# Kernel optimization log

Hardware: AMD Instinct MI355X
Metric: run time of the kernel (lower is better)

The kernel has to match this reference:

```python
import jax, jax.numpy as jnp
import numpy as np

# Dims: C = 8*8*4 = 256 input channels, O = 8*8*8 = 512 output channels,
# space_rank = 4, TT ranks = (4, 16, 16).

def setup_inputs() -> dict:
    key = jax.random.key(0)
    ks = jax.random.split(key, 6)
    inp = jax.random.normal(ks[0], (32, 256, 32, 32), dtype=jnp.float32)
    # space_factor: (space_rank, 1, kH, kW)
    space_factor = jax.random.normal(ks[1], (4, 1, 3, 3), dtype=jnp.float32) * 0.3
    # factors[i]: (in_i, rank_i, rank_{i+1}, out_i)
    factor0 = jax.random.normal(ks[2], (8, 4, 16, 8), dtype=jnp.float32) * 0.1
    factor1 = jax.random.normal(ks[3], (8, 16, 16, 8), dtype=jnp.float32) * 0.08
    # last_factor: (in_last, rank_last, out_last)
    last_factor = jax.random.normal(ks[4], (4, 16, 8), dtype=jnp.float32) * 0.1
    bias = jax.random.uniform(ks[5], (512,), dtype=jnp.float32, minval=-0.02, maxval=0.02)
    return {"input": inp, "space_factor": space_factor, "factor0": factor0,
            "factor1": factor1, "last_factor": last_factor, "bias": bias}


def reference(input, space_factor, factor0, factor1, last_factor, bias):
    B, C, H, W = input.shape
    sr = space_factor.shape[0]
    # Depthwise conv: each of the C channels convolved with the same
    # `space_rank` filters (torch repeat along out-channel dim + groups=C).
    w = jnp.tile(space_factor, (C, 1, 1, 1))  # (C*sr, 1, kH, kW)
    y = jax.lax.conv_general_dilated(
        input, w, window_strides=(1, 1), padding=[(1, 1), (1, 1)],
        feature_group_count=C,
        dimension_numbers=("NCHW", "OIHW", "NCHW"))  # (B, C*sr, H', W')
    Hp, Wp = y.shape[2], y.shape[3]
    # (B, n0, n1, n2, sr, H', W') with (n0,n1,n2) = input_chanel_shape
    t = y.reshape(B, 8, 8, 4, sr, Hp, Wp)
    # Contract the tiny TT cores first (optimal order found by tn.contractors.optimal):
    # chain: (n0, n1, n2, r0, o0, o1, o2) -- only ~0.5M elements.
    chain = jnp.einsum("apqx,bqry,crz->abcpxyz", factor0, factor1, last_factor)
    # One big contraction over (n0, n1, n2, r0): effectively a GEMM
    # (B*H'*W', C*sr) x (C*sr, O).
    out = jnp.einsum("nabcphw,abcpxyz->nxyzhw", t, chain)
    out = out.reshape(B, 512, Hp, Wp)
    return out + bias[None, :, None, None]
```

## Files before the change

### kernel.cpp

```cpp
#include <hip/hip_runtime.h>

typedef unsigned short ushort_t;
typedef __attribute__((ext_vector_type(8))) short bf16x8;
typedef __attribute__((ext_vector_type(8))) unsigned short ushort8;
typedef __attribute__((ext_vector_type(4))) float f32x4;

__device__ __forceinline__ unsigned short f2bf(float f) {
  union { float f; unsigned u; } x; x.f = f;
  unsigned r = x.u + 0x7FFFu + ((x.u >> 16) & 1u);
  return (unsigned short)(r >> 16);
}

__global__ __launch_bounds__(256) void chain_kernel(const float* __restrict__ f0,
                                                    const float* __restrict__ f1,
                                                    const float* __restrict__ lf,
                                                    ushort_t* __restrict__ chainT) {
  __shared__ float gs[512];
  int o = blockIdx.x;
  int z = o & 7, y = (o >> 3) & 7, x = o >> 6;
  int tid = threadIdx.x;
  #pragma unroll
  for (int i = 0; i < 2; ++i) {
    int e = tid + i * 256;
    int c = e & 3, q = (e >> 2) & 15, b = e >> 6;
    float s = 0.f;
    #pragma unroll
    for (int r = 0; r < 16; ++r)
      s += f1[((b * 16 + q) * 16 + r) * 8 + y] * lf[(c * 16 + r) * 8 + z];
    gs[e] = s;
  }
  __syncthreads();
  #pragma unroll
  for (int j = 0; j < 4; ++j) {
    int k = tid + j * 256;
    int p = k & 3, c = (k >> 2) & 3, b = (k >> 4) & 7, a = k >> 7;
    float s = 0.f;
    #pragma unroll
    for (int q = 0; q < 16; ++q)
      s += f0[((a * 4 + p) * 16 + q) * 8 + x] * gs[(b * 16 + q) * 4 + c];
    chainT[(size_t)o * 1024 + k] = f2bf(s);
  }
}

__global__ __launch_bounds__(256) void conv_kernel(const float* __restrict__ in,
                                                   const float* __restrict__ sf,
                                                   ushort_t* __restrict__ t) {
  __shared__ float in_lds[64][244];
  __shared__ float sf_l[36];
  int bid = blockIdx.x;
  int cq = bid & 3, h4 = (bid >> 2) & 7, n = bid >> 5;
  int h0 = h4 * 4;
  int tid = threadIdx.x;
  if (tid < 36) sf_l[tid] = sf[tid];
  for (int e = tid; e < 384; e += 256) {
    int ch = e / 6, r = e % 6;
    in_lds[ch][r * 40 + 3] = 0.f;
    in_lds[ch][r * 40 + 36] = 0.f;
  }
  const float* inb = in + ((size_t)n * 256 + cq * 64) * 1024;
  #pragma unroll
  for (int i = 0; i < 12; ++i) {
    int e = tid + i * 256;
    int ch = e / 48, rem = e % 48;
    int r = rem >> 3, w4 = rem & 7;
    int hh = h0 - 1 + r;
    float4 v = make_float4(0.f, 0.f, 0.f, 0.f);
    if (hh >= 0 && hh < 32)
      v = *(const float4*)&inb[(size_t)ch * 1024 + hh * 32 + w4 * 4];
    *(float4*)&in_lds[ch][r * 40 + 4 + w4 * 4] = v;
  }
  __syncthreads();
  float sfr[36];
  #pragma unroll
  for (int i = 0; i < 36; ++i) sfr[i] = sf_l[i];
  int w = tid >> 3, gg = tid & 7;
  size_t m0 = (size_t)n * 1024 + (size_t)h0 * 32 + w;
  #pragma unroll
  for (int j = 0; j < 4; ++j) {
    float acc[4][2][4];
    #pragma unroll
    for (int b = 0; b < 2; ++b) {
      int ch = j * 16 + gg * 2 + b;
      float vals[6][3];
      #pragma unroll
      for (int r = 0; r < 6; ++r)
        #pragma unroll
        for (int dw = 0; dw < 3; ++dw)
          vals[r][dw] = in_lds[ch][r * 40 + 3 + w + dw];
      #pragma unroll
      for (int hh = 0; hh < 4; ++hh)
        #pragma unroll
        for (int p = 0; p < 4; ++p) {
          float s = 0.f;
          #pragma unroll
          for (int dr = 0; dr < 3; ++dr)
            #pragma unroll
            for (int dw = 0; dw < 3; ++dw)
              s += vals[hh + dr][dw] * sfr[p * 9 + dr * 3 + dw];
          acc[hh][b][p] = s;
        }
    }
    #pragma unroll
    for (int hh = 0; hh < 4; ++hh) {
      ushort8 outv;
      #pragma unroll
      for (int b = 0; b < 2; ++b)
        #pragma unroll
        for (int p = 0; p < 4; ++p) outv[b * 4 + p] = f2bf(acc[hh][b][p]);
      *(ushort8*)&t[(m0 + hh * 32) * 1024 + (size_t)(cq * 256 + j * 64 + gg * 8)] = outv;
    }
  }
}

#define AS1 __attribute__((address_space(1)))
#define AS3 __attribute__((address_space(3)))
#define BARRIER  __builtin_amdgcn_s_barrier()
#define LGKMCNT0 asm volatile("s_waitcnt lgkmcnt(0)" ::: "memory")
#define VMCNT4   asm volatile("s_waitcnt vmcnt(4)" ::: "memory")
#define VMCNT0   asm volatile("s_waitcnt vmcnt(0)" ::: "memory")

__global__ __launch_bounds__(512, 2) void gemm_kernel(const ushort_t* __restrict__ tA,
                                                      const ushort_t* __restrict__ tB,
                                                      const float* __restrict__ bias,
                                                      float* __restrict__ out) {
  __shared__ __align__(16) ushort_t smem[65536];
  int tid = threadIdx.x;
  int bid = blockIdx.x;
  int wg = (bid & 7) * 32 + (bid >> 3);
  int tile_m = (wg >> 1) * 256;
  int tile_n = (wg & 1) * 256;

  int lane = tid & 63, wv = tid >> 6;
  int wm2 = wv >> 2, wn4 = wv & 3;
  int lr = lane & 15, kg = lane >> 4;
  int kph0 = ((kg * 8) ^ ((lane & 7) * 8));
  int kph1 = ((32 + kg * 8) ^ ((lane & 7) * 8));
  int arow = wm2 * 128 + lr;
  int brow = wn4 * 64 + lr;

  int srow = tid >> 3;
  int scol = ((tid & 7) ^ (srow & 7)) * 8;
  const ushort_t* sA = tA + (size_t)(tile_m + srow) * 1024 + scol;
  const ushort_t* sB = tB + (size_t)(tile_n + srow) * 1024 + scol;

#define STAGE_A(buf, koff, h)                                                                  \
  __builtin_amdgcn_global_load_lds((const AS1 void*)(sA + (size_t)((h)*128) * 1024 + (koff)),  \
      (AS3 void*)&smem[(buf)*16384 + (h)*8192 + tid*8], 16, 0, 0);                             \
  __builtin_amdgcn_global_load_lds((const AS1 void*)(sA + (size_t)((h)*128+64) * 1024 + (koff)),\
      (AS3 void*)&smem[(buf)*16384 + (h)*8192 + 4096 + tid*8], 16, 0, 0);
#define STAGE_B(buf, koff, h)                                                                  \
  __builtin_amdgcn_global_load_lds((const AS1 void*)(sB + (size_t)((h)*128) * 1024 + (koff)),  \
      (AS3 void*)&smem[32768 + (buf)*16384 + (h)*8192 + tid*8], 16, 0, 0);                     \
  __builtin_amdgcn_global_load_lds((const AS1 void*)(sB + (size_t)((h)*128+64) * 1024 + (koff)),\
      (AS3 void*)&smem[32768 + (buf)*16384 + (h)*8192 + 4096 + tid*8], 16, 0, 0);

#define READ_A(dst, mbase, buf)                                                                \
  _Pragma("unroll")                                                                            \
  for (int mf = 0; mf < 4; ++mf) {                                                             \
    dst[mf][0] = *(const bf16x8*)&smem[(buf)*16384 + (arow + (mbase) + mf*16)*64 + kph0];      \
    dst[mf][1] = *(const bf16x8*)&smem[(buf)*16384 + (arow + (mbase) + mf*16)*64 + kph1];      \
  }
#define READ_B(dst, nbase, buf)                                                                \
  _Pragma("unroll")                                                                            \
  for (int nf = 0; nf < 2; ++nf) {                                                             \
    dst[nf][0] = *(const bf16x8*)&smem[32768 + (buf)*16384 + (brow + (nbase) + nf*16)*64 + kph0];\
    dst[nf][1] = *(const bf16x8*)&smem[32768 + (buf)*16384 + (brow + (nbase) + nf*16)*64 + kph1];\
  }
#define Q_MFMA(AF, BF, MB, NB)                                                                 \
  __builtin_amdgcn_s_setprio(1);                                                              \
  _Pragma("unroll")                                                                            \
  for (int mf = 0; mf < 4; ++mf)                                                               \
    _Pragma("unroll")                                                                          \
    for (int nf = 0; nf < 2; ++nf)                                                             \
      _Pragma("unroll")                                                                        \
      for (int ks = 0; ks < 2; ++ks)                                                           \
        acc[(MB) + mf][(NB) + nf] = __builtin_amdgcn_mfma_f32_16x16x32_bf16(                   \
            AF[mf][ks], BF[nf][ks], acc[(MB) + mf][(NB) + nf], 0, 0, 0);                       \
  __builtin_amdgcn_s_setprio(0);

  f32x4 acc[8][4];
  #pragma unroll
  for (int i = 0; i < 8; ++i)
    #pragma unroll
    for (int j = 0; j < 4; ++j) acc[i][j] = (f32x4){0.f, 0.f, 0.f, 0.f};

  bf16x8 a1[4][2], a2[4][2], b1[2][2], b2[2][2];

  STAGE_A(0, 0, 0) STAGE_A(0, 0, 1) STAGE_B(0, 0, 0) STAGE_B(0, 0, 1)
  STAGE_A(1, 64, 0) STAGE_A(1, 64, 1)
  VMCNT4; BARRIER;

#define ITER(I_, FULL)                                                                         \
  {                                                                                            \
    int k1 = (2*(I_)+1)*64, k2 = (2*(I_)+2)*64, k3 = (2*(I_)+3)*64;                            \
                       \
    READ_A(a1, 0, 0) READ_B(b1, 0, 0)                                                          \
    STAGE_B(1, k1, 0)                                                                          \
    Q_MFMA(a1, b1, 0, 0) BARRIER;                                                              \
                                 \
    READ_B(b2, 32, 0) READ_A(a2, 64, 0)                                                        \
    STAGE_B(1, k1, 1)                                                                          \
    Q_MFMA(a1, b2, 0, 2) LGKMCNT0; BARRIER;                                                    \
                          \
    if (FULL) { STAGE_A(0, k2, 0) }                                                            \
    Q_MFMA(a2, b2, 4, 2) BARRIER;                                                              \
                                        \
    if (FULL) { STAGE_A(0, k2, 1) }                                                            \
    Q_MFMA(a2, b1, 4, 0)                                                                       \
    if (FULL) { VMCNT4; } else { VMCNT0; }                                                     \
    BARRIER;                                                                                   \
                                                                                       \
    READ_A(a1, 0, 1) READ_B(b1, 0, 1)                                                          \
    if (FULL) { STAGE_B(0, k2, 0) }                                                            \
    Q_MFMA(a1, b1, 0, 0) BARRIER;                                                              \
                                                                                       \
    READ_B(b2, 32, 1) READ_A(a2, 64, 1)                                                        \
    if (FULL) { STAGE_B(0, k2, 1) }                                                            \
    Q_MFMA(a1, b2, 0, 2) LGKMCNT0; BARRIER;                                                    \
                                                                                       \
    if (FULL) { STAGE_A(1, k3, 0) }                                                            \
    Q_MFMA(a2, b2, 4, 2) BARRIER;                                                              \
                                   \
    if (FULL) { STAGE_A(1, k3, 1) }                                                            \
    Q_MFMA(a2, b1, 4, 0)                                                                       \
    if (FULL) { VMCNT4; }                                                                      \
    BARRIER;                                                                                   \
  }

  for (int I = 0; I < 7; ++I) ITER(I, 1)
  ITER(7, 0)
#undef ITER

  #pragma unroll
  for (int mf = 0; mf < 8; ++mf)
    #pragma unroll
    for (int nf = 0; nf < 4; ++nf) {
      int m = tile_m + wm2 * 128 + mf * 16 + kg * 4;
      int o = tile_n + wn4 * 64 + nf * 16 + lr;
      float bv = bias[o];
      f32x4 v = acc[mf][nf];
      v[0] += bv; v[1] += bv; v[2] += bv; v[3] += bv;
      *(f32x4*)&out[(size_t)(m >> 10) * 524288 + (size_t)o * 1024 + (size_t)(m & 1023)] = v;
    }
}

extern "C" void kernel_launch(void* const* d_in, const int* in_sizes, int n_in,
                              void* d_out, int out_size, void* d_ws, size_t ws_size,
                              hipStream_t stream) {
  (void)in_sizes; (void)n_in; (void)out_size; (void)ws_size;
  const float* in   = (const float*)d_in[0];
  const float* sf   = (const float*)d_in[1];
  const float* f0   = (const float*)d_in[2];
  const float* f1   = (const float*)d_in[3];
  const float* lf   = (const float*)d_in[4];
  const float* bias = (const float*)d_in[5];
  float* out = (float*)d_out;

  char* ws = (char*)d_ws;
  ushort_t* t      = (ushort_t*)ws;
  ushort_t* chainT = (ushort_t*)(ws + 67108864);

  hipLaunchKernelGGL(chain_kernel, dim3(512),  dim3(256), 0, stream, f0, f1, lf, chainT);
  hipLaunchKernelGGL(conv_kernel,  dim3(1024), dim3(256), 0, stream, in, sf, t);
  hipLaunchKernelGGL(gemm_kernel,  dim3(256),  dim3(512), 0, stream, t, chainT, bias, out);
}
```

Baseline: 75.07 us.

## Retile depthwise conv blocks to 16 channels by 8 rows with coalesced-lane mapping

The conv kernel now gives each block 16 channels and 8 output rows instead of 64 channels and 4 rows, launching twice as many blocks with a much smaller LDS footprint. Threads map w to the lane index, so neighbouring lanes read adjacent LDS columns, and each thread reuses a 10-row register window across 8 output rows, cutting halo reloads. Outputs are packed into 16-byte stores per row. The risk is that row stores now span 32 distinct pixels per wave with 16-byte chunks, which may coalesce worse in the channel-last bf16 layout.

```diff
diff --git a/kernel.cpp b/kernel.cpp
--- a/kernel.cpp
+++ b/kernel.cpp
@@ -45,23 +45,22 @@
 __global__ __launch_bounds__(256) void conv_kernel(const float* __restrict__ in,
                                                    const float* __restrict__ sf,
                                                    ushort_t* __restrict__ t) {
-  __shared__ float in_lds[64][244];
+  __shared__ float in_lds[16][404];
   __shared__ float sf_l[36];
   int bid = blockIdx.x;
-  int cq = bid & 3, h4 = (bid >> 2) & 7, n = bid >> 5;
-  int h0 = h4 * 4;
+  int cg = bid & 15, hg = (bid >> 4) & 3, n = bid >> 6;
+  int h0 = hg * 8;
   int tid = threadIdx.x;
   if (tid < 36) sf_l[tid] = sf[tid];
-  for (int e = tid; e < 384; e += 256) {
-    int ch = e / 6, r = e % 6;
-    in_lds[ch][r * 40 + 3] = 0.f;
-    in_lds[ch][r * 40 + 36] = 0.f;
-  }
-  const float* inb = in + ((size_t)n * 256 + cq * 64) * 1024;
-  #pragma unroll
-  for (int i = 0; i < 12; ++i) {
+  for (int e = tid; e < 320; e += 256) {
+    int ch = e / 20, rr = e % 20;
+    in_lds[ch][(rr >> 1) * 40 + 3 + (rr & 1) * 33] = 0.f;
+  }
+  const float* inb = in + ((size_t)n * 256 + cg * 16) * 1024;
+  #pragma unroll
+  for (int i = 0; i < 5; ++i) {
     int e = tid + i * 256;
-    int ch = e / 48, rem = e % 48;
+    int ch = e / 80, rem = e % 80;
     int r = rem >> 3, w4 = rem & 7;
     int hh = h0 - 1 + r;
     float4 v = make_float4(0.f, 0.f, 0.f, 0.f);
@@ -73,42 +72,39 @@
   float sfr[36];
   #pragma unroll
   for (int i = 0; i < 36; ++i) sfr[i] = sf_l[i];
-  int w = tid >> 3, gg = tid & 7;
+  int w = tid & 31, sub = tid >> 5;
   size_t m0 = (size_t)n * 1024 + (size_t)h0 * 32 + w;
-  #pragma unroll
-  for (int j = 0; j < 4; ++j) {
-    float acc[4][2][4];
-    #pragma unroll
-    for (int b = 0; b < 2; ++b) {
-      int ch = j * 16 + gg * 2 + b;
-      float vals[6][3];
+  unsigned pw[8][4];
+  #pragma unroll
+  for (int b = 0; b < 2; ++b) {
+    int ch = sub * 2 + b;
+    float vals[10][3];
+    #pragma unroll
+    for (int r = 0; r < 10; ++r)
       #pragma unroll
-      for (int r = 0; r < 6; ++r)
+      for (int dw = 0; dw < 3; ++dw)
+        vals[r][dw] = in_lds[ch][r * 40 + 3 + w + dw];
+    #pragma unroll
+    for (int j = 0; j < 8; ++j) {
+      float s0 = 0.f, s1 = 0.f, s2 = 0.f, s3 = 0.f;
+      #pragma unroll
+      for (int dr = 0; dr < 3; ++dr)
         #pragma unroll
-        for (int dw = 0; dw < 3; ++dw)
-          vals[r][dw] = in_lds[ch][r * 40 + 3 + w + dw];
-      #pragma unroll
-      for (int hh = 0; hh < 4; ++hh)
-        #pragma unroll
-        for (int p = 0; p < 4; ++p) {
-          float s = 0.f;
-          #pragma unroll
-          for (int dr = 0; dr < 3; ++dr)
-            #pragma unroll
-            for (int dw = 0; dw < 3; ++dw)
-              s += vals[hh + dr][dw] * sfr[p * 9 + dr * 3 + dw];
-          acc[hh][b][p] = s;
+        for (int dw = 0; dw < 3; ++dw) {
+          float tv = vals[j + dr][dw];
+          s0 += tv * sfr[0 * 9 + dr * 3 + dw];
+          s1 += tv * sfr[1 * 9 + dr * 3 + dw];
+          s2 += tv * sfr[2 * 9 + dr * 3 + dw];
+          s3 += tv * sfr[3 * 9 + dr * 3 + dw];
         }
+      pw[j][b * 2 + 0] = (unsigned)f2bf(s0) | ((unsigned)f2bf(s1) << 16);
+      pw[j][b * 2 + 1] = (unsigned)f2bf(s2) | ((unsigned)f2bf(s3) << 16);
     }
-    #pragma unroll
-    for (int hh = 0; hh < 4; ++hh) {
-      ushort8 outv;
-      #pragma unroll
-      for (int b = 0; b < 2; ++b)
-        #pragma unroll
-        for (int p = 0; p < 4; ++p) outv[b * 4 + p] = f2bf(acc[hh][b][p]);
-      *(ushort8*)&t[(m0 + hh * 32) * 1024 + (size_t)(cq * 256 + j * 64 + gg * 8)] = outv;
-    }
+  }
+  #pragma unroll
+  for (int j = 0; j < 8; ++j) {
+    uint4 pk; pk.x = pw[j][0]; pk.y = pw[j][1]; pk.z = pw[j][2]; pk.w = pw[j][3];
+    *(uint4*)&t[(m0 + (size_t)j * 32) * 1024 + (size_t)(cg * 64 + sub * 8)] = pk;
   }
 }
 
@@ -193,34 +189,26 @@
 #define ITER(I_, FULL)                                                                         \
   {                                                                                            \
     int k1 = (2*(I_)+1)*64, k2 = (2*(I_)+2)*64, k3 = (2*(I_)+3)*64;                            \
-                       \
     READ_A(a1, 0, 0) READ_B(b1, 0, 0)                                                          \
     STAGE_B(1, k1, 0)                                                                          \
     Q_MFMA(a1, b1, 0, 0) BARRIER;                                                              \
-                                 \
     READ_B(b2, 32, 0) READ_A(a2, 64, 0)                                                        \
     STAGE_B(1, k1, 1)                                                                          \
     Q_MFMA(a1, b2, 0, 2) LGKMCNT0; BARRIER;                                                    \
-                          \
     if (FULL) { STAGE_A(0, k2, 0) }                                                            \
     Q_MFMA(a2, b2, 4, 2) BARRIER;                                                              \
-                                        \
     if (FULL) { STAGE_A(0, k2, 1) }                                                            \
     Q_MFMA(a2, b1, 4, 0)                                                                       \
     if (FULL) { VMCNT4; } else { VMCNT0; }                                                     \
     BARRIER;                                                                                   \
-                                                                                       \
     READ_A(a1, 0, 1) READ_B(b1, 0, 1)                                                          \
     if (FULL) { STAGE_B(0, k2, 0) }                                                            \
     Q_MFMA(a1, b1, 0, 0) BARRIER;                                                              \
-                                                                                       \
     READ_B(b2, 32, 1) READ_A(a2, 64, 1)                                                        \
     if (FULL) { STAGE_B(0, k2, 1) }                                                            \
     Q_MFMA(a1, b2, 0, 2) LGKMCNT0; BARRIER;                                                    \
-                                                                                       \
     if (FULL) { STAGE_A(1, k3, 0) }                                                            \
     Q_MFMA(a2, b2, 4, 2) BARRIER;                                                              \
-                                   \
     if (FULL) { STAGE_A(1, k3, 1) }                                                            \
     Q_MFMA(a2, b1, 4, 0)                                                                       \
     if (FULL) { VMCNT4; }                                                                      \
@@ -261,6 +249,6 @@
   ushort_t* chainT = (ushort_t*)(ws + 67108864);
 
   hipLaunchKernelGGL(chain_kernel, dim3(512),  dim3(256), 0, stream, f0, f1, lf, chainT);
-  hipLaunchKernelGGL(conv_kernel,  dim3(1024), dim3(256), 0, stream, in, sf, t);
+  hipLaunchKernelGGL(conv_kernel,  dim3(2048), dim3(256), 0, stream, in, sf, t);
   hipLaunchKernelGGL(gemm_kernel,  dim3(256),  dim3(512), 0, stream, t, chainT, bias, out);
 }
```

Result: faster. 71.00 us (-5.4%).
